# Optimization experiments

Measured on AMD Instinct MI355X. Metric: run time of the kernel, lower is better.

## Reference

```python
import jax, jax.numpy as jnp
import numpy as np

INT8_MAX = 127.0
EQN = 'bsd,df->bsf'


def _quantize(x, axes):
    """Symmetric int8 abs-max quantization over contraction axes.

    Returns (q, scale) with q in [-127, 127] (stored fp32) and scale shaped
    with keepdims so that q * scale ~ x.
    """
    absmax = jnp.max(jnp.abs(x), axis=axes, keepdims=True)
    scale = absmax / INT8_MAX
    scale = jnp.where(scale == 0.0, jnp.ones_like(scale), scale)
    q = jnp.clip(jnp.round(x / scale), -INT8_MAX, INT8_MAX)
    return q, scale


def setup_inputs() -> dict:
    key = jax.random.key(0)
    k1, k2 = jax.random.split(key)
    lhs = jax.random.normal(k1, (4, 2048, 4096), dtype=jnp.float32)
    rhs = jax.random.normal(k2, (4096, 16384), dtype=jnp.float32)
    return {"lhs": lhs, "rhs": rhs}


def reference(lhs, rhs):
    # AQT quantized einsum 'bsd,df->bsf':
    #   per-(b,s)-row int8 quantization of lhs over contraction axis d,
    #   per-column (f) int8 quantization of rhs over contraction axis d,
    #   low-precision matmul, then dequantize by the outer product of scales.
    q_lhs, s_lhs = _quantize(lhs, axes=(2,))   # q:[b,s,d], s:[b,s,1]
    q_rhs, s_rhs = _quantize(rhs, axes=(0,))   # q:[d,f],  s:[1,f]
    acc = jnp.einsum(EQN, q_lhs, q_rhs)        # int-valued accumulation in fp32
    # dequant: scales factor out of the contraction
    return acc * s_lhs * s_rhs[None]           # [b,s,f]
```

## Files before the change

### kernel.cpp

```cpp
#include <hip/hip_runtime.h>
#include <hip/hip_bf16.h>
#include <stdint.h>

#define M_TOT 8192
#define N_TOT 16384
#define K_TOT 4096

typedef int v4i __attribute__((ext_vector_type(4)));
typedef int v16i __attribute__((ext_vector_type(16)));

__device__ __forceinline__ float fix_scale(float s) { return s == 0.0f ? 1.0f : s; }

__device__ __forceinline__ void gload_lds16(const void* g, void* l) {
    __builtin_amdgcn_global_load_lds((__attribute__((address_space(1))) void*)g,
                                     (__attribute__((address_space(3))) void*)l,
                                     16, 0, 0);
}

__device__ __forceinline__ int8_t quant1(float x, float scale) {
    float r = fminf(127.0f, fmaxf(-127.0f, rintf(x / scale)));
    return (int8_t)(int)r;
}

__device__ __forceinline__ unsigned pack4(float4 v, float scale) {
    unsigned b0 = (unsigned char)quant1(v.x, scale);
    unsigned b1 = (unsigned char)quant1(v.y, scale);
    unsigned b2 = (unsigned char)quant1(v.z, scale);
    unsigned b3 = (unsigned char)quant1(v.w, scale);
    return b0 | (b1 << 8) | (b2 << 16) | (b3 << 24);
}


__global__ __launch_bounds__(256) void k_quant_lhs(const float* __restrict__ x,
                                                   int8_t* __restrict__ qt,
                                                   float* __restrict__ s) {
    const int row = blockIdx.x;
    const int t = threadIdx.x;
    const float4* xr = (const float4*)(x + (size_t)row * K_TOT);
    float4 v[4];
    float m = 0.0f;
#pragma unroll
    for (int i = 0; i < 4; ++i) {
        v[i] = xr[t * 4 + i];
        m = fmaxf(m, fmaxf(fmaxf(fabsf(v[i].x), fabsf(v[i].y)),
                           fmaxf(fabsf(v[i].z), fabsf(v[i].w))));
    }
#pragma unroll
    for (int off = 32; off; off >>= 1) m = fmaxf(m, __shfl_xor(m, off));
    __shared__ float wmax[4];
    if ((t & 63) == 0) wmax[t >> 6] = m;
    __syncthreads();
    m = fmaxf(fmaxf(wmax[0], wmax[1]), fmaxf(wmax[2], wmax[3]));
    const float scale = fix_scale(m / 127.0f);
    if (t == 0) s[row] = scale;

    v4i w;
#pragma unroll
    for (int i = 0; i < 4; ++i) w[i] = (int)pack4(v[i], scale);

    const int mt = row >> 8, mb = (row >> 5) & 7, r = row & 31;
    const int kt = t >> 2, s2 = (t >> 1) & 1, h = t & 1;
    const size_t gidx = (size_t)(mt * 64 + kt) * 1024 + (size_t)((mb * 2 + s2) * 64 + h * 32 + r);
    ((v4i*)qt)[gidx] = w;
}

__global__ __launch_bounds__(256) void k_rhs_absmax(const float* __restrict__ rhs,
                                                    unsigned* __restrict__ amax) {
    const int f = blockIdx.x * 256 + threadIdx.x;
    const int d0 = blockIdx.y * 256;
    const float* p = rhs + (size_t)d0 * N_TOT + f;
    float m = 0.0f;
#pragma unroll 4
    for (int d = 0; d < 256; ++d)
        m = fmaxf(m, fabsf(p[(size_t)d * N_TOT]));
    atomicMax(amax + f, __float_as_uint(m));
}

__global__ __launch_bounds__(256) void k_rhs_scale(const unsigned* __restrict__ amax,
                                                   float* __restrict__ s) {
    const int f = blockIdx.x * 256 + threadIdx.x;
    s[f] = fix_scale(__uint_as_float(amax[f]) / 127.0f);
}

__global__ __launch_bounds__(256) void k_quant_rhs_t(const float* __restrict__ rhs,
                                                     const float* __restrict__ s,
                                                     int8_t* __restrict__ qt) {
    const int f0 = blockIdx.x * 64;
    const int d0 = blockIdx.y * 64;
    const int t = threadIdx.x;
    __shared__ float sc[64];
    __shared__ alignas(16) int8_t tile[64][64];
    if (t < 64) sc[t] = s[f0 + t];
    __syncthreads();
    const int fl = (t & 15) * 4;
    const int rl = t >> 4;
#pragma unroll
    for (int i = 0; i < 4; ++i) {
        const int dl = i * 16 + rl;
        float4 v = *(const float4*)(rhs + (size_t)(d0 + dl) * N_TOT + f0 + fl);
        tile[fl + 0][dl] = quant1(v.x, sc[fl + 0]);
        tile[fl + 1][dl] = quant1(v.y, sc[fl + 1]);
        tile[fl + 2][dl] = quant1(v.z, sc[fl + 2]);
        tile[fl + 3][dl] = quant1(v.w, sc[fl + 3]);
    }
    __syncthreads();
    const int nb_l = t >> 7, s2 = (t >> 6) & 1, h = (t >> 5) & 1, r = t & 31;
    const int col_local = nb_l * 32 + r;
    const int kb16 = s2 * 2 + h;
    const int nt = f0 >> 8;
    const int nb = ((f0 >> 5) & 7) + nb_l;
    const int kt = d0 >> 6;
    const size_t gidx = (size_t)(nt * 64 + kt) * 1024 + (size_t)((nb * 2 + s2) * 64 + h * 32 + r);
    ((v4i*)qt)[gidx] = *(const v4i*)&tile[col_local][kb16 * 16];
}

#define BM 256
#define BN 256
#define BK 64
#define NKT (K_TOT / BK)

__global__ __launch_bounds__(512, 2) void k_gemm(const int8_t* __restrict__ qA,
                                                 const int8_t* __restrict__ qB,
                                                 const float* __restrict__ sA,
                                                 const float* __restrict__ sB,
                                                 float* __restrict__ C) {
    __shared__ alignas(1024) int8_t lds[3][32768];

    const int bid = blockIdx.x;
    const int scc = bid >> 6;
    const int ii = bid & 63;
    const int mt = ii & 31;
    const int ntile = (scc << 1) | (ii >> 5);
    const int bm0 = mt << 8;
    const int bn0 = ntile << 8;

    const int tid = threadIdx.x;
    const int wave = tid >> 6;
    const int lane = tid & 63;
    const int wm = (wave >> 2) * 128;
    const int wn = (wave & 3) * 64;

    const int8_t* aBase = qA + (size_t)mt * (64 * 16384);
    const int8_t* bBase = qB + (size_t)ntile * (64 * 16384);

    const int aoff = (wave >> 2) * 4 * 2048 + lane * 16;
    const int boff = 16384 + (wave & 3) * 2 * 2048 + lane * 16;

    v16i acc[4][2];
#pragma unroll
    for (int f = 0; f < 4; ++f)
#pragma unroll
        for (int n = 0; n < 2; ++n)
#pragma unroll
            for (int e = 0; e < 16; ++e) acc[f][n][e] = 0;

    auto stage_half = [&](int kt, int h) {
        const int b = kt % 3;
        const int loff = h * 8192 + tid * 16;
        const int8_t* src = (h < 2) ? (aBase + (size_t)kt * 16384 + h * 8192 + tid * 16)
                                    : (bBase + (size_t)kt * 16384 + (h - 2) * 8192 + tid * 16);
        gload_lds16(src, &lds[b][loff]);
    };

    stage_half(0, 0); stage_half(0, 1); stage_half(0, 2); stage_half(0, 3);
    stage_half(1, 0); stage_half(1, 1); stage_half(1, 2); stage_half(1, 3);
    asm volatile("s_waitcnt vmcnt(4)" ::: "memory");
    __builtin_amdgcn_s_barrier();

    for (int kt = 0; kt < NKT; ++kt) {
        const int8_t* a = &lds[kt % 3][0];
        const bool st = (kt + 2 < NKT);
        v4i af[2], bf0[2], bf1[2];

        af[0] = *(const v4i*)(a + aoff + 0 * 2048);
        af[1] = *(const v4i*)(a + aoff + 1 * 2048);
        bf0[0] = *(const v4i*)(a + boff + 0 * 2048);
        bf0[1] = *(const v4i*)(a + boff + 1 * 2048);
        if (st) stage_half(kt + 2, 0);
        __builtin_amdgcn_s_barrier();
        asm volatile("s_waitcnt lgkmcnt(0)" ::: "memory");
        __builtin_amdgcn_s_setprio(1);
        acc[0][0] = __builtin_amdgcn_mfma_i32_32x32x32_i8(af[0], bf0[0], acc[0][0], 0, 0, 0);
        acc[0][1] = __builtin_amdgcn_mfma_i32_32x32x32_i8(af[0], bf0[1], acc[0][1], 0, 0, 0);
        acc[1][0] = __builtin_amdgcn_mfma_i32_32x32x32_i8(af[1], bf0[0], acc[1][0], 0, 0, 0);
        acc[1][1] = __builtin_amdgcn_mfma_i32_32x32x32_i8(af[1], bf0[1], acc[1][1], 0, 0, 0);
        __builtin_amdgcn_s_setprio(0);
        __builtin_amdgcn_s_barrier();

        af[0] = *(const v4i*)(a + aoff + 2 * 2048);
        af[1] = *(const v4i*)(a + aoff + 3 * 2048);
        if (st) stage_half(kt + 2, 1);
        __builtin_amdgcn_s_barrier();
        asm volatile("s_waitcnt lgkmcnt(0)" ::: "memory");
        __builtin_amdgcn_s_setprio(1);
        acc[2][0] = __builtin_amdgcn_mfma_i32_32x32x32_i8(af[0], bf0[0], acc[2][0], 0, 0, 0);
        acc[2][1] = __builtin_amdgcn_mfma_i32_32x32x32_i8(af[0], bf0[1], acc[2][1], 0, 0, 0);
        acc[3][0] = __builtin_amdgcn_mfma_i32_32x32x32_i8(af[1], bf0[0], acc[3][0], 0, 0, 0);
        acc[3][1] = __builtin_amdgcn_mfma_i32_32x32x32_i8(af[1], bf0[1], acc[3][1], 0, 0, 0);
        __builtin_amdgcn_s_setprio(0);
        __builtin_amdgcn_s_barrier();

        af[0] = *(const v4i*)(a + aoff + 0 * 2048 + 1024);
        af[1] = *(const v4i*)(a + aoff + 1 * 2048 + 1024);
        bf1[0] = *(const v4i*)(a + boff + 0 * 2048 + 1024);
        bf1[1] = *(const v4i*)(a + boff + 1 * 2048 + 1024);
        if (st) stage_half(kt + 2, 2);
        __builtin_amdgcn_s_barrier();
        asm volatile("s_waitcnt lgkmcnt(0)" ::: "memory");
        __builtin_amdgcn_s_setprio(1);
        acc[0][0] = __builtin_amdgcn_mfma_i32_32x32x32_i8(af[0], bf1[0], acc[0][0], 0, 0, 0);
        acc[0][1] = __builtin_amdgcn_mfma_i32_32x32x32_i8(af[0], bf1[1], acc[0][1], 0, 0, 0);
        acc[1][0] = __builtin_amdgcn_mfma_i32_32x32x32_i8(af[1], bf1[0], acc[1][0], 0, 0, 0);
        acc[1][1] = __builtin_amdgcn_mfma_i32_32x32x32_i8(af[1], bf1[1], acc[1][1], 0, 0, 0);
        __builtin_amdgcn_s_setprio(0);
        __builtin_amdgcn_s_barrier();

        af[0] = *(const v4i*)(a + aoff + 2 * 2048 + 1024);
        af[1] = *(const v4i*)(a + aoff + 3 * 2048 + 1024);
        if (st) stage_half(kt + 2, 3);
        __builtin_amdgcn_s_barrier();
        asm volatile("s_waitcnt lgkmcnt(0)" ::: "memory");
        __builtin_amdgcn_s_setprio(1);
        acc[2][0] = __builtin_amdgcn_mfma_i32_32x32x32_i8(af[0], bf1[0], acc[2][0], 0, 0, 0);
        acc[2][1] = __builtin_amdgcn_mfma_i32_32x32x32_i8(af[0], bf1[1], acc[2][1], 0, 0, 0);
        acc[3][0] = __builtin_amdgcn_mfma_i32_32x32x32_i8(af[1], bf1[0], acc[3][0], 0, 0, 0);
        acc[3][1] = __builtin_amdgcn_mfma_i32_32x32x32_i8(af[1], bf1[1], acc[3][1], 0, 0, 0);
        __builtin_amdgcn_s_setprio(0);
        if (kt + 2 < NKT)      asm volatile("s_waitcnt vmcnt(4)" ::: "memory");
        else if (kt + 1 < NKT) asm volatile("s_waitcnt vmcnt(0)" ::: "memory");
        __builtin_amdgcn_s_barrier();
    }

    const int cc0 = lane & 31;
    const int rbase = (lane >> 5) * 4;
#pragma unroll
    for (int f = 0; f < 4; ++f) {
#pragma unroll
        for (int r = 0; r < 16; ++r) {
            const int gr = bm0 + wm + f * 32 + (r & 3) + 8 * (r >> 2) + rbase;
            const float sa = sA[gr];
            float* crow = C + (size_t)gr * N_TOT + bn0 + wn;
#pragma unroll
            for (int n = 0; n < 2; ++n)
                crow[n * 32 + cc0] = (float)acc[f][n][r] * sa * sB[bn0 + wn + n * 32 + cc0];
        }
    }
}

extern "C" void kernel_launch(void* const* d_in, const int* in_sizes, int n_in,
                              void* d_out, int out_size, void* d_ws, size_t ws_size,
                              hipStream_t stream) {
    const float* lhs = (const float*)d_in[0];
    const float* rhs = (const float*)d_in[1];
    float* out = (float*)d_out;
    char* ws = (char*)d_ws;

    int8_t* qA = (int8_t*)ws;
    int8_t* qB = (int8_t*)(ws + (size_t)33554432);
    float* sA = (float*)(ws + (size_t)33554432 + 67108864);
    float* sB = sA + M_TOT;
    unsigned* amax = (unsigned*)(sB + N_TOT);

    hipMemsetAsync(amax, 0, N_TOT * sizeof(unsigned), stream);

    k_quant_lhs<<<M_TOT, 256, 0, stream>>>(lhs, qA, sA);
    k_rhs_absmax<<<dim3(N_TOT / 256, K_TOT / 256), 256, 0, stream>>>(rhs, amax);
    k_rhs_scale<<<N_TOT / 256, 256, 0, stream>>>(amax, sB);
    k_quant_rhs_t<<<dim3(N_TOT / 64, K_TOT / 64), 256, 0, stream>>>(rhs, sB, qB);
    k_gemm<<<(M_TOT / BM) * (N_TOT / BN), 512, 0, stream>>>(qA, qB, sA, sB, out);
}
```

Measured before the change: 749.8 us.

## Load B fragments directly from global into registers, keep only A in LDS

B operand tiles are no longer staged through LDS; each wave loads its own B fragments straight from global memory into registers one k-tile ahead, using a two-buffer register ping-pong (loop unrolled by two). LDS now holds only the A tiles, halving shared-memory footprint and LDS read traffic. The trade-off is that B is fetched redundantly by the two wave rows, and global load latency is now exposed directly to the register pipeline. The vmcnt accounting is also changed, so ordering must stay correct with the mixed global and LDS-targeted loads.

```diff
diff --git a/kernel.cpp b/kernel.cpp
--- a/kernel.cpp
+++ b/kernel.cpp
@@ -119,12 +119,14 @@
 #define BK 64
 #define NKT (K_TOT / BK)
 
+#define MFMA_I8(A, B, Cc) __builtin_amdgcn_mfma_i32_32x32x32_i8((A), (B), (Cc), 0, 0, 0)
+
 __global__ __launch_bounds__(512, 2) void k_gemm(const int8_t* __restrict__ qA,
                                                  const int8_t* __restrict__ qB,
                                                  const float* __restrict__ sA,
                                                  const float* __restrict__ sB,
                                                  float* __restrict__ C) {
-    __shared__ alignas(1024) int8_t lds[3][32768];
+    __shared__ alignas(1024) int8_t Asmem[3][16384];
 
     const int bid = blockIdx.x;
     const int scc = bid >> 6;
@@ -141,10 +143,9 @@
     const int wn = (wave & 3) * 64;
 
     const int8_t* aBase = qA + (size_t)mt * (64 * 16384);
-    const int8_t* bBase = qB + (size_t)ntile * (64 * 16384);
-
-    const int aoff = (wave >> 2) * 4 * 2048 + lane * 16;
-    const int boff = 16384 + (wave & 3) * 2 * 2048 + lane * 16;
+    const int8_t* bBase = qB + (size_t)ntile * (64 * 16384) + (wave & 3) * 4096 + lane * 16;
+
+    const int aoff = (wave >> 2) * 8192 + lane * 16;
 
     v16i acc[4][2];
 #pragma unroll
@@ -154,81 +155,93 @@
 #pragma unroll
             for (int e = 0; e < 16; ++e) acc[f][n][e] = 0;
 
-    auto stage_half = [&](int kt, int h) {
-        const int b = kt % 3;
-        const int loff = h * 8192 + tid * 16;
-        const int8_t* src = (h < 2) ? (aBase + (size_t)kt * 16384 + h * 8192 + tid * 16)
-                                    : (bBase + (size_t)kt * 16384 + (h - 2) * 8192 + tid * 16);
-        gload_lds16(src, &lds[b][loff]);
+    auto stageA = [&](int kt, int h) {
+        gload_lds16(aBase + (size_t)kt * 16384 + h * 8192 + tid * 16,
+                    &Asmem[kt % 3][h * 8192 + tid * 16]);
     };
 
-    stage_half(0, 0); stage_half(0, 1); stage_half(0, 2); stage_half(0, 3);
-    stage_half(1, 0); stage_half(1, 1); stage_half(1, 2); stage_half(1, 3);
-    asm volatile("s_waitcnt vmcnt(4)" ::: "memory");
+    v4i b0[2][2], b1[2][2];
+
+    stageA(0, 0); stageA(0, 1);
+    b0[0][0] = *(const v4i*)(bBase);
+    b0[0][1] = *(const v4i*)(bBase + 1024);
+    b0[1][0] = *(const v4i*)(bBase + 2048);
+    b0[1][1] = *(const v4i*)(bBase + 3072);
+    stageA(1, 0); stageA(1, 1);
+    asm volatile("s_waitcnt vmcnt(2)" ::: "memory");
     __builtin_amdgcn_s_barrier();
 
-    for (int kt = 0; kt < NKT; ++kt) {
-        const int8_t* a = &lds[kt % 3][0];
-        const bool st = (kt + 2 < NKT);
-        v4i af[2], bf0[2], bf1[2];
+    auto body = [&](int kt, v4i (&bc)[2][2], v4i (&bn_)[2][2]) {
+        const int8_t* a = &Asmem[kt % 3][0];
+        const int8_t* bsrc = bBase + (size_t)(kt + 1) * 16384;
+        const bool stA = (kt + 2 < NKT);
+        const bool ldB = (kt + 1 < NKT);
+        v4i af[2];
 
         af[0] = *(const v4i*)(a + aoff + 0 * 2048);
         af[1] = *(const v4i*)(a + aoff + 1 * 2048);
-        bf0[0] = *(const v4i*)(a + boff + 0 * 2048);
-        bf0[1] = *(const v4i*)(a + boff + 1 * 2048);
-        if (st) stage_half(kt + 2, 0);
-        __builtin_amdgcn_s_barrier();
-        asm volatile("s_waitcnt lgkmcnt(0)" ::: "memory");
-        __builtin_amdgcn_s_setprio(1);
-        acc[0][0] = __builtin_amdgcn_mfma_i32_32x32x32_i8(af[0], bf0[0], acc[0][0], 0, 0, 0);
-        acc[0][1] = __builtin_amdgcn_mfma_i32_32x32x32_i8(af[0], bf0[1], acc[0][1], 0, 0, 0);
-        acc[1][0] = __builtin_amdgcn_mfma_i32_32x32x32_i8(af[1], bf0[0], acc[1][0], 0, 0, 0);
-        acc[1][1] = __builtin_amdgcn_mfma_i32_32x32x32_i8(af[1], bf0[1], acc[1][1], 0, 0, 0);
+        if (ldB) {
+            bn_[0][0] = *(const v4i*)(bsrc);
+            bn_[0][1] = *(const v4i*)(bsrc + 1024);
+        }
+        __builtin_amdgcn_s_barrier();
+        asm volatile("s_waitcnt lgkmcnt(0)" ::: "memory");
+        __builtin_amdgcn_s_setprio(1);
+        acc[0][0] = MFMA_I8(af[0], bc[0][0], acc[0][0]);
+        acc[0][1] = MFMA_I8(af[0], bc[1][0], acc[0][1]);
+        acc[1][0] = MFMA_I8(af[1], bc[0][0], acc[1][0]);
+        acc[1][1] = MFMA_I8(af[1], bc[1][0], acc[1][1]);
         __builtin_amdgcn_s_setprio(0);
         __builtin_amdgcn_s_barrier();
 
         af[0] = *(const v4i*)(a + aoff + 2 * 2048);
         af[1] = *(const v4i*)(a + aoff + 3 * 2048);
-        if (st) stage_half(kt + 2, 1);
-        __builtin_amdgcn_s_barrier();
-        asm volatile("s_waitcnt lgkmcnt(0)" ::: "memory");
-        __builtin_amdgcn_s_setprio(1);
-        acc[2][0] = __builtin_amdgcn_mfma_i32_32x32x32_i8(af[0], bf0[0], acc[2][0], 0, 0, 0);
-        acc[2][1] = __builtin_amdgcn_mfma_i32_32x32x32_i8(af[0], bf0[1], acc[2][1], 0, 0, 0);
-        acc[3][0] = __builtin_amdgcn_mfma_i32_32x32x32_i8(af[1], bf0[0], acc[3][0], 0, 0, 0);
-        acc[3][1] = __builtin_amdgcn_mfma_i32_32x32x32_i8(af[1], bf0[1], acc[3][1], 0, 0, 0);
+        if (ldB) {
+            bn_[1][0] = *(const v4i*)(bsrc + 2048);
+            bn_[1][1] = *(const v4i*)(bsrc + 3072);
+        }
+        __builtin_amdgcn_s_barrier();
+        asm volatile("s_waitcnt lgkmcnt(0)" ::: "memory");
+        __builtin_amdgcn_s_setprio(1);
+        acc[2][0] = MFMA_I8(af[0], bc[0][0], acc[2][0]);
+        acc[2][1] = MFMA_I8(af[0], bc[1][0], acc[2][1]);
+        acc[3][0] = MFMA_I8(af[1], bc[0][0], acc[3][0]);
+        acc[3][1] = MFMA_I8(af[1], bc[1][0], acc[3][1]);
         __builtin_amdgcn_s_setprio(0);
         __builtin_amdgcn_s_barrier();
 
         af[0] = *(const v4i*)(a + aoff + 0 * 2048 + 1024);
         af[1] = *(const v4i*)(a + aoff + 1 * 2048 + 1024);
-        bf1[0] = *(const v4i*)(a + boff + 0 * 2048 + 1024);
-        bf1[1] = *(const v4i*)(a + boff + 1 * 2048 + 1024);
-        if (st) stage_half(kt + 2, 2);
-        __builtin_amdgcn_s_barrier();
-        asm volatile("s_waitcnt lgkmcnt(0)" ::: "memory");
-        __builtin_amdgcn_s_setprio(1);
-        acc[0][0] = __builtin_amdgcn_mfma_i32_32x32x32_i8(af[0], bf1[0], acc[0][0], 0, 0, 0);
-        acc[0][1] = __builtin_amdgcn_mfma_i32_32x32x32_i8(af[0], bf1[1], acc[0][1], 0, 0, 0);
-        acc[1][0] = __builtin_amdgcn_mfma_i32_32x32x32_i8(af[1], bf1[0], acc[1][0], 0, 0, 0);
-        acc[1][1] = __builtin_amdgcn_mfma_i32_32x32x32_i8(af[1], bf1[1], acc[1][1], 0, 0, 0);
+        if (stA) stageA(kt + 2, 0);
+        __builtin_amdgcn_s_barrier();
+        asm volatile("s_waitcnt lgkmcnt(0)" ::: "memory");
+        __builtin_amdgcn_s_setprio(1);
+        acc[0][0] = MFMA_I8(af[0], bc[0][1], acc[0][0]);
+        acc[0][1] = MFMA_I8(af[0], bc[1][1], acc[0][1]);
+        acc[1][0] = MFMA_I8(af[1], bc[0][1], acc[1][0]);
+        acc[1][1] = MFMA_I8(af[1], bc[1][1], acc[1][1]);
         __builtin_amdgcn_s_setprio(0);
         __builtin_amdgcn_s_barrier();
 
         af[0] = *(const v4i*)(a + aoff + 2 * 2048 + 1024);
         af[1] = *(const v4i*)(a + aoff + 3 * 2048 + 1024);
-        if (st) stage_half(kt + 2, 3);
-        __builtin_amdgcn_s_barrier();
-        asm volatile("s_waitcnt lgkmcnt(0)" ::: "memory");
-        __builtin_amdgcn_s_setprio(1);
-        acc[2][0] = __builtin_amdgcn_mfma_i32_32x32x32_i8(af[0], bf1[0], acc[2][0], 0, 0, 0);
-        acc[2][1] = __builtin_amdgcn_mfma_i32_32x32x32_i8(af[0], bf1[1], acc[2][1], 0, 0, 0);
-        acc[3][0] = __builtin_amdgcn_mfma_i32_32x32x32_i8(af[1], bf1[0], acc[3][0], 0, 0, 0);
-        acc[3][1] = __builtin_amdgcn_mfma_i32_32x32x32_i8(af[1], bf1[1], acc[3][1], 0, 0, 0);
-        __builtin_amdgcn_s_setprio(0);
-        if (kt + 2 < NKT)      asm volatile("s_waitcnt vmcnt(4)" ::: "memory");
+        if (stA) stageA(kt + 2, 1);
+        __builtin_amdgcn_s_barrier();
+        asm volatile("s_waitcnt lgkmcnt(0)" ::: "memory");
+        __builtin_amdgcn_s_setprio(1);
+        acc[2][0] = MFMA_I8(af[0], bc[0][1], acc[2][0]);
+        acc[2][1] = MFMA_I8(af[0], bc[1][1], acc[2][1]);
+        acc[3][0] = MFMA_I8(af[1], bc[0][1], acc[3][0]);
+        acc[3][1] = MFMA_I8(af[1], bc[1][1], acc[3][1]);
+        __builtin_amdgcn_s_setprio(0);
+        if (kt + 2 < NKT)      asm volatile("s_waitcnt vmcnt(2)" ::: "memory");
         else if (kt + 1 < NKT) asm volatile("s_waitcnt vmcnt(0)" ::: "memory");
-        __builtin_amdgcn_s_barrier();
+        if (kt + 1 < NKT) __builtin_amdgcn_s_barrier();
+    };
+
+    for (int kt = 0; kt < NKT; kt += 2) {
+        body(kt, b0, b1);
+        body(kt + 1, b1, b0);
     }
 
     const int cc0 = lane & 31;
```

Result: slower. 998.5 us (+33.2%).

## Switch int8 GEMM to 16x16x64 MFMA with new operand layout and 4-stage LDS ring

Applied to the files above, without the earlier changes.

Replaces the 32x32x32 int8 MFMA tiling with 16x16x64 MFMAs, so each wave holds an 8x4 grid of small accumulators. The quantization kernels write A and B in a new 16-row group layout to match these operands. The K loop is unrolled by two over a 4-buffer LDS ring that stages tiles two steps ahead. The separate rhs scale kernel is folded into the rhs quantize kernel to save a launch. The main risks are worse coalescing in the 16-wide epilogue stores and larger LDS use.

```diff
diff --git a/kernel.cpp b/kernel.cpp
--- a/kernel.cpp
+++ b/kernel.cpp
@@ -7,7 +7,6 @@
 #define K_TOT 4096
 
 typedef int v4i __attribute__((ext_vector_type(4)));
-typedef int v16i __attribute__((ext_vector_type(16)));
 
 __device__ __forceinline__ float fix_scale(float s) { return s == 0.0f ? 1.0f : s; }
 
@@ -58,9 +57,9 @@
 #pragma unroll
     for (int i = 0; i < 4; ++i) w[i] = (int)pack4(v[i], scale);
 
-    const int mt = row >> 8, mb = (row >> 5) & 7, r = row & 31;
-    const int kt = t >> 2, s2 = (t >> 1) & 1, h = t & 1;
-    const size_t gidx = (size_t)(mt * 64 + kt) * 1024 + (size_t)((mb * 2 + s2) * 64 + h * 32 + r);
+    const int mt = row >> 8, fg = (row >> 4) & 15, r = row & 15;
+    const int kt = t >> 2, kb = t & 3;
+    const size_t gidx = ((size_t)(mt * 64 + kt) * 16 + fg) * 64 + kb * 16 + r;
     ((v4i*)qt)[gidx] = w;
 }
 
@@ -76,21 +75,20 @@
     atomicMax(amax + f, __float_as_uint(m));
 }
 
-__global__ __launch_bounds__(256) void k_rhs_scale(const unsigned* __restrict__ amax,
-                                                   float* __restrict__ s) {
-    const int f = blockIdx.x * 256 + threadIdx.x;
-    s[f] = fix_scale(__uint_as_float(amax[f]) / 127.0f);
-}
-
 __global__ __launch_bounds__(256) void k_quant_rhs_t(const float* __restrict__ rhs,
-                                                     const float* __restrict__ s,
+                                                     const unsigned* __restrict__ amax,
+                                                     float* __restrict__ sB,
                                                      int8_t* __restrict__ qt) {
     const int f0 = blockIdx.x * 64;
     const int d0 = blockIdx.y * 64;
     const int t = threadIdx.x;
     __shared__ float sc[64];
     __shared__ alignas(16) int8_t tile[64][64];
-    if (t < 64) sc[t] = s[f0 + t];
+    if (t < 64) {
+        const float scale = fix_scale(__uint_as_float(amax[f0 + t]) / 127.0f);
+        sc[t] = scale;
+        if (blockIdx.y == 0) sB[f0 + t] = scale;
+    }
     __syncthreads();
     const int fl = (t & 15) * 4;
     const int rl = t >> 4;
@@ -104,27 +102,27 @@
         tile[fl + 3][dl] = quant1(v.w, sc[fl + 3]);
     }
     __syncthreads();
-    const int nb_l = t >> 7, s2 = (t >> 6) & 1, h = (t >> 5) & 1, r = t & 31;
-    const int col_local = nb_l * 32 + r;
-    const int kb16 = s2 * 2 + h;
-    const int nt = f0 >> 8;
-    const int nb = ((f0 >> 5) & 7) + nb_l;
+    const int cl = t >> 2, kb = t & 3;
+    const int col = f0 + cl;
+    const int nt = col >> 8, fg = (col >> 4) & 15, r = col & 15;
     const int kt = d0 >> 6;
-    const size_t gidx = (size_t)(nt * 64 + kt) * 1024 + (size_t)((nb * 2 + s2) * 64 + h * 32 + r);
-    ((v4i*)qt)[gidx] = *(const v4i*)&tile[col_local][kb16 * 16];
+    const size_t gidx = ((size_t)(nt * 64 + kt) * 16 + fg) * 64 + kb * 16 + r;
+    ((v4i*)qt)[gidx] = *(const v4i*)&tile[cl][kb * 16];
 }
 
 #define BM 256
 #define BN 256
 #define BK 64
 #define NKT (K_TOT / BK)
+
+#define MFMA16(A, B, Cc) __builtin_amdgcn_mfma_i32_16x16x64_i8((A), (B), (Cc), 0, 0, 0)
 
 __global__ __launch_bounds__(512, 2) void k_gemm(const int8_t* __restrict__ qA,
                                                  const int8_t* __restrict__ qB,
                                                  const float* __restrict__ sA,
                                                  const float* __restrict__ sB,
                                                  float* __restrict__ C) {
-    __shared__ alignas(1024) int8_t lds[3][32768];
+    __shared__ alignas(1024) int8_t lds[4][32768];
 
     const int bid = blockIdx.x;
     const int scc = bid >> 6;
@@ -143,23 +141,23 @@
     const int8_t* aBase = qA + (size_t)mt * (64 * 16384);
     const int8_t* bBase = qB + (size_t)ntile * (64 * 16384);
 
-    const int aoff = (wave >> 2) * 4 * 2048 + lane * 16;
-    const int boff = 16384 + (wave & 3) * 2 * 2048 + lane * 16;
-
-    v16i acc[4][2];
-#pragma unroll
-    for (int f = 0; f < 4; ++f)
-#pragma unroll
-        for (int n = 0; n < 2; ++n)
-#pragma unroll
-            for (int e = 0; e < 16; ++e) acc[f][n][e] = 0;
+    const int aoff = (wave >> 2) * 8192 + lane * 16;
+    const int boff = 16384 + (wave & 3) * 4096 + lane * 16;
+
+    v4i acc[8][4];
+#pragma unroll
+    for (int f = 0; f < 8; ++f)
+#pragma unroll
+        for (int n = 0; n < 4; ++n) {
+            v4i z = {0, 0, 0, 0};
+            acc[f][n] = z;
+        }
 
     auto stage_half = [&](int kt, int h) {
-        const int b = kt % 3;
-        const int loff = h * 8192 + tid * 16;
+        const int b = kt & 3;
         const int8_t* src = (h < 2) ? (aBase + (size_t)kt * 16384 + h * 8192 + tid * 16)
                                     : (bBase + (size_t)kt * 16384 + (h - 2) * 8192 + tid * 16);
-        gload_lds16(src, &lds[b][loff]);
+        gload_lds16(src, &lds[b][h * 8192 + tid * 16]);
     };
 
     stage_half(0, 0); stage_half(0, 1); stage_half(0, 2); stage_half(0, 3);
@@ -167,82 +165,91 @@
     asm volatile("s_waitcnt vmcnt(4)" ::: "memory");
     __builtin_amdgcn_s_barrier();
 
-    for (int kt = 0; kt < NKT; ++kt) {
-        const int8_t* a = &lds[kt % 3][0];
+    for (int kt = 0; kt < NKT; kt += 2) {
+        const int8_t* a0 = &lds[kt & 3][0];
+        const int8_t* a1 = &lds[(kt + 1) & 3][0];
         const bool st = (kt + 2 < NKT);
-        v4i af[2], bf0[2], bf1[2];
-
-        af[0] = *(const v4i*)(a + aoff + 0 * 2048);
-        af[1] = *(const v4i*)(a + aoff + 1 * 2048);
-        bf0[0] = *(const v4i*)(a + boff + 0 * 2048);
-        bf0[1] = *(const v4i*)(a + boff + 1 * 2048);
-        if (st) stage_half(kt + 2, 0);
-        __builtin_amdgcn_s_barrier();
-        asm volatile("s_waitcnt lgkmcnt(0)" ::: "memory");
-        __builtin_amdgcn_s_setprio(1);
-        acc[0][0] = __builtin_amdgcn_mfma_i32_32x32x32_i8(af[0], bf0[0], acc[0][0], 0, 0, 0);
-        acc[0][1] = __builtin_amdgcn_mfma_i32_32x32x32_i8(af[0], bf0[1], acc[0][1], 0, 0, 0);
-        acc[1][0] = __builtin_amdgcn_mfma_i32_32x32x32_i8(af[1], bf0[0], acc[1][0], 0, 0, 0);
-        acc[1][1] = __builtin_amdgcn_mfma_i32_32x32x32_i8(af[1], bf0[1], acc[1][1], 0, 0, 0);
-        __builtin_amdgcn_s_setprio(0);
-        __builtin_amdgcn_s_barrier();
-
-        af[0] = *(const v4i*)(a + aoff + 2 * 2048);
-        af[1] = *(const v4i*)(a + aoff + 3 * 2048);
-        if (st) stage_half(kt + 2, 1);
-        __builtin_amdgcn_s_barrier();
-        asm volatile("s_waitcnt lgkmcnt(0)" ::: "memory");
-        __builtin_amdgcn_s_setprio(1);
-        acc[2][0] = __builtin_amdgcn_mfma_i32_32x32x32_i8(af[0], bf0[0], acc[2][0], 0, 0, 0);
-        acc[2][1] = __builtin_amdgcn_mfma_i32_32x32x32_i8(af[0], bf0[1], acc[2][1], 0, 0, 0);
-        acc[3][0] = __builtin_amdgcn_mfma_i32_32x32x32_i8(af[1], bf0[0], acc[3][0], 0, 0, 0);
-        acc[3][1] = __builtin_amdgcn_mfma_i32_32x32x32_i8(af[1], bf0[1], acc[3][1], 0, 0, 0);
-        __builtin_amdgcn_s_setprio(0);
-        __builtin_amdgcn_s_barrier();
-
-        af[0] = *(const v4i*)(a + aoff + 0 * 2048 + 1024);
-        af[1] = *(const v4i*)(a + aoff + 1 * 2048 + 1024);
-        bf1[0] = *(const v4i*)(a + boff + 0 * 2048 + 1024);
-        bf1[1] = *(const v4i*)(a + boff + 1 * 2048 + 1024);
-        if (st) stage_half(kt + 2, 2);
-        __builtin_amdgcn_s_barrier();
-        asm volatile("s_waitcnt lgkmcnt(0)" ::: "memory");
-        __builtin_amdgcn_s_setprio(1);
-        acc[0][0] = __builtin_amdgcn_mfma_i32_32x32x32_i8(af[0], bf1[0], acc[0][0], 0, 0, 0);
-        acc[0][1] = __builtin_amdgcn_mfma_i32_32x32x32_i8(af[0], bf1[1], acc[0][1], 0, 0, 0);
-        acc[1][0] = __builtin_amdgcn_mfma_i32_32x32x32_i8(af[1], bf1[0], acc[1][0], 0, 0, 0);
-        acc[1][1] = __builtin_amdgcn_mfma_i32_32x32x32_i8(af[1], bf1[1], acc[1][1], 0, 0, 0);
-        __builtin_amdgcn_s_setprio(0);
-        __builtin_amdgcn_s_barrier();
-
-        af[0] = *(const v4i*)(a + aoff + 2 * 2048 + 1024);
-        af[1] = *(const v4i*)(a + aoff + 3 * 2048 + 1024);
-        if (st) stage_half(kt + 2, 3);
-        __builtin_amdgcn_s_barrier();
-        asm volatile("s_waitcnt lgkmcnt(0)" ::: "memory");
-        __builtin_amdgcn_s_setprio(1);
-        acc[2][0] = __builtin_amdgcn_mfma_i32_32x32x32_i8(af[0], bf1[0], acc[2][0], 0, 0, 0);
-        acc[2][1] = __builtin_amdgcn_mfma_i32_32x32x32_i8(af[0], bf1[1], acc[2][1], 0, 0, 0);
-        acc[3][0] = __builtin_amdgcn_mfma_i32_32x32x32_i8(af[1], bf1[0], acc[3][0], 0, 0, 0);
-        acc[3][1] = __builtin_amdgcn_mfma_i32_32x32x32_i8(af[1], bf1[1], acc[3][1], 0, 0, 0);
-        __builtin_amdgcn_s_setprio(0);
-        if (kt + 2 < NKT)      asm volatile("s_waitcnt vmcnt(4)" ::: "memory");
-        else if (kt + 1 < NKT) asm volatile("s_waitcnt vmcnt(0)" ::: "memory");
-        __builtin_amdgcn_s_barrier();
-    }
-
-    const int cc0 = lane & 31;
-    const int rbase = (lane >> 5) * 4;
-#pragma unroll
-    for (int f = 0; f < 4; ++f) {
-#pragma unroll
-        for (int r = 0; r < 16; ++r) {
-            const int gr = bm0 + wm + f * 32 + (r & 3) + 8 * (r >> 2) + rbase;
-            const float sa = sA[gr];
-            float* crow = C + (size_t)gr * N_TOT + bn0 + wn;
-#pragma unroll
-            for (int n = 0; n < 2; ++n)
-                crow[n * 32 + cc0] = (float)acc[f][n][r] * sa * sB[bn0 + wn + n * 32 + cc0];
+        v4i A[8], B[4];
+
+#pragma unroll
+        for (int f = 0; f < 4; ++f) A[f] = *(const v4i*)(a0 + aoff + f * 1024);
+#pragma unroll
+        for (int n = 0; n < 4; ++n) B[n] = *(const v4i*)(a0 + boff + n * 1024);
+        if (st) { stage_half(kt + 2, 0); stage_half(kt + 2, 1); }
+        __builtin_amdgcn_s_barrier();
+        asm volatile("s_waitcnt lgkmcnt(0)" ::: "memory");
+        __builtin_amdgcn_s_setprio(1);
+#pragma unroll
+        for (int f = 0; f < 4; ++f)
+#pragma unroll
+            for (int n = 0; n < 4; ++n)
+                acc[f][n] = MFMA16(A[f], B[n], acc[f][n]);
+        __builtin_amdgcn_s_setprio(0);
+        __builtin_amdgcn_s_barrier();
+
+#pragma unroll
+        for (int f = 0; f < 4; ++f) A[4 + f] = *(const v4i*)(a0 + aoff + (4 + f) * 1024);
+        if (st) { stage_half(kt + 2, 2); stage_half(kt + 2, 3); }
+        __builtin_amdgcn_s_barrier();
+        asm volatile("s_waitcnt lgkmcnt(0)" ::: "memory");
+        __builtin_amdgcn_s_setprio(1);
+#pragma unroll
+        for (int f = 0; f < 4; ++f)
+#pragma unroll
+            for (int n = 0; n < 4; ++n)
+                acc[4 + f][n] = MFMA16(A[4 + f], B[n], acc[4 + f][n]);
+        __builtin_amdgcn_s_setprio(0);
+        if (st) asm volatile("s_waitcnt vmcnt(4)" ::: "memory");
+        else    asm volatile("s_waitcnt vmcnt(0)" ::: "memory");
+        __builtin_amdgcn_s_barrier();
+
+#pragma unroll
+        for (int f = 0; f < 4; ++f) A[f] = *(const v4i*)(a1 + aoff + f * 1024);
+#pragma unroll
+        for (int n = 0; n < 4; ++n) B[n] = *(const v4i*)(a1 + boff + n * 1024);
+        if (st) { stage_half(kt + 3, 0); stage_half(kt + 3, 1); }
+        __builtin_amdgcn_s_barrier();
+        asm volatile("s_waitcnt lgkmcnt(0)" ::: "memory");
+        __builtin_amdgcn_s_setprio(1);
+#pragma unroll
+        for (int f = 0; f < 4; ++f)
+#pragma unroll
+            for (int n = 0; n < 4; ++n)
+                acc[f][n] = MFMA16(A[f], B[n], acc[f][n]);
+        __builtin_amdgcn_s_setprio(0);
+        __builtin_amdgcn_s_barrier();
+
+#pragma unroll
+        for (int f = 0; f < 4; ++f) A[4 + f] = *(const v4i*)(a1 + aoff + (4 + f) * 1024);
+        if (st) { stage_half(kt + 3, 2); stage_half(kt + 3, 3); }
+        __builtin_amdgcn_s_barrier();
+        asm volatile("s_waitcnt lgkmcnt(0)" ::: "memory");
+        __builtin_amdgcn_s_setprio(1);
+#pragma unroll
+        for (int f = 0; f < 4; ++f)
+#pragma unroll
+            for (int n = 0; n < 4; ++n)
+                acc[4 + f][n] = MFMA16(A[4 + f], B[n], acc[4 + f][n]);
+        __builtin_amdgcn_s_setprio(0);
+        if (st) asm volatile("s_waitcnt vmcnt(4)" ::: "memory");
+        __builtin_amdgcn_s_barrier();
+    }
+
+    const int cc0 = lane & 15;
+    const int rbase = (lane >> 4) * 4;
+#pragma unroll
+    for (int f = 0; f < 8; ++f) {
+        const int gr0 = bm0 + wm + f * 16 + rbase;
+        float sa[4];
+#pragma unroll
+        for (int r = 0; r < 4; ++r) sa[r] = sA[gr0 + r];
+#pragma unroll
+        for (int n = 0; n < 4; ++n) {
+            const int gc = bn0 + wn + n * 16 + cc0;
+            const float sb = sB[gc];
+#pragma unroll
+            for (int r = 0; r < 4; ++r)
+                C[(size_t)(gr0 + r) * N_TOT + gc] = (float)acc[f][n][r] * sa[r] * sb;
         }
     }
 }
@@ -265,7 +272,6 @@
 
     k_quant_lhs<<<M_TOT, 256, 0, stream>>>(lhs, qA, sA);
     k_rhs_absmax<<<dim3(N_TOT / 256, K_TOT / 256), 256, 0, stream>>>(rhs, amax);
-    k_rhs_scale<<<N_TOT / 256, 256, 0, stream>>>(amax, sB);
-    k_quant_rhs_t<<<dim3(N_TOT / 64, K_TOT / 64), 256, 0, stream>>>(rhs, sB, qB);
+    k_quant_rhs_t<<<dim3(N_TOT / 64, K_TOT / 64), 256, 0, stream>>>(rhs, amax, sB, qB);
     k_gemm<<<(M_TOT / BM) * (N_TOT / BN), 512, 0, stream>>>(qA, qB, sA, sB, out);
 }
```

Result: no change. 737.4 us (-1.7%).
